# Performance work log

Measured on AMD Instinct MI355X. Metric: run time of the kernel, lower is better.

The kernel has to match this reference:

```python
import jax, jax.numpy as jnp
import numpy as np

N = 100000      # nodes
E = 1600000     # edges (avg degree 16)
F_NODE = 128
F_EDGE = 32
H = 32          # hidden size hard-coded in module


def setup_inputs() -> dict:
    key = jax.random.key(0)
    ks = jax.random.split(key, 16)
    w = lambda k, s: jax.random.normal(k, s, jnp.float32) * 0.05
    z = lambda n: jnp.zeros((n,), jnp.float32)
    return {
        "x": jax.random.normal(ks[0], (N, F_NODE), jnp.float32),
        "edge_index": jax.random.randint(ks[1], (2, E), 0, N),
        "edge_attr": jax.random.normal(ks[2], (E, F_EDGE), jnp.float32),
        "W_node": w(ks[3], (F_NODE, H)), "b_node": z(H),
        "W_edge": w(ks[4], (F_EDGE, H)), "b_edge": z(H),
        # TGCN: three GCNConv(32,32) gate convs + three Linear(64,32)
        "Wg_z": w(ks[5], (H, H)), "bg_z": z(H),
        "Wg_r": w(ks[6], (H, H)), "bg_r": z(H),
        "Wg_h": w(ks[7], (H, H)), "bg_h": z(H),
        "Wl_z": w(ks[8], (2 * H, H)), "bl_z": z(H),
        "Wl_r": w(ks[9], (2 * H, H)), "bl_r": z(H),
        "Wl_h": w(ks[10], (2 * H, H)), "bl_h": z(H),
        "W_out": w(ks[11], (3 * H, 1)), "b_out": z(1),
    }


def _gcn(x, row, col, dis, W, b, n):
    # GCNConv with added self-loops and symmetric normalization.
    xw = x @ W                                        # [N, H]
    msg = (dis[row] * dis[col])[:, None] * xw[row]    # [E, H]
    agg = jax.ops.segment_sum(msg, col, num_segments=n)
    agg = agg + (dis * dis)[:, None] * xw             # self-loop term
    return agg + b


def reference(x, edge_index, edge_attr, W_node, b_node, W_edge, b_edge,
              Wg_z, bg_z, Wg_r, bg_r, Wg_h, bg_h,
              Wl_z, bl_z, Wl_r, bl_r, Wl_h, bl_h, W_out, b_out):
    n = x.shape[0]
    row, col = edge_index[0], edge_index[1]
    x_enc = jax.nn.relu(x @ W_node + b_node)          # [N, 32]
    e_enc = jax.nn.relu(edge_attr @ W_edge + b_edge)  # [E, 32]

    # degree (target side) including self loop
    deg = jax.ops.segment_sum(jnp.ones_like(col, dtype=x.dtype), col,
                              num_segments=n) + 1.0
    dis = jax.lax.rsqrt(deg)

    h0 = jnp.zeros_like(x_enc)                        # TGCN initial state H=None -> zeros
    Z = jax.nn.sigmoid(
        jnp.concatenate([_gcn(x_enc, row, col, dis, Wg_z, bg_z, n), h0], 1) @ Wl_z + bl_z)
    R = jax.nn.sigmoid(
        jnp.concatenate([_gcn(x_enc, row, col, dis, Wg_r, bg_r, n), h0], 1) @ Wl_r + bl_r)
    Ht = jnp.tanh(
        jnp.concatenate([_gcn(x_enc, row, col, dis, Wg_h, bg_h, n), h0 * R], 1) @ Wl_h + bl_h)
    h = Z * h0 + (1.0 - Z) * Ht                       # [N, 32]

    # edge-level gather-concat + final linear -> [E, 1]
    edge_feat = jnp.concatenate([h[row], h[col], e_enc], axis=1)  # [E, 96]
    return edge_feat @ W_out + b_out
```

## Files before the change

kernel.cpp:

```cpp
#include <hip/hip_runtime.h>
#include <hip/hip_bf16.h>

#define F_NODE 128
#define BINCAP 64

__device__ __forceinline__ float bflo(unsigned int v) {
    return __uint_as_float(v << 16);
}
__device__ __forceinline__ float bfhi(unsigned int v) {
    return __uint_as_float(v & 0xffff0000u);
}
__device__ __forceinline__ unsigned short bfpack(float f) {
    __hip_bfloat16 b = __float2bfloat16(f);
    return *reinterpret_cast<unsigned short*>(&b);
}

__global__ void k_prep(const float* __restrict__ Wn,
                       const float* __restrict__ Wgz, const float* __restrict__ Wgh,
                       const float* __restrict__ Wlz, const float* __restrict__ Wlh,
                       const float* __restrict__ bgz, const float* __restrict__ bgh,
                       const float* __restrict__ blz, const float* __restrict__ blh,
                       const float* __restrict__ We,
                       float* __restrict__ Wnt, float* __restrict__ Mt,
                       float* __restrict__ cvec, float* __restrict__ Wet) {
    int tid = threadIdx.x;
    for (int j = tid; j < 32 * 128; j += 256) {
        int f = j >> 7, k = j & 127;
        Wnt[j] = Wn[k * 32 + f];
    }
    for (int j = tid; j < 64 * 32; j += 256) {
        int f2 = j >> 5, k = j & 31, f = f2 & 31;
        const float* G = (f2 < 32) ? Wgz : Wgh;
        const float* L = (f2 < 32) ? Wlz : Wlh;
        float s = 0.f;
        for (int q = 0; q < 32; ++q) s += G[k * 32 + q] * L[q * 32 + f];
        Mt[j] = s;
    }
    for (int j = tid; j < 64; j += 256) {
        int f = j & 31;
        const float* L  = (j < 32) ? Wlz : Wlh;
        const float* bg = (j < 32) ? bgz : bgh;
        const float* bl = (j < 32) ? blz : blh;
        float s = bl[f];
        for (int q = 0; q < 32; ++q) s += bg[q] * L[q * 32 + f];
        cvec[j] = s;
    }
    for (int j = tid; j < 32 * 32; j += 256) {
        int f = j >> 5, k = j & 31;
        Wet[j] = We[k * 32 + f];
    }
}

__global__ __launch_bounds__(256) void k_fat(
        const int* __restrict__ row, const int* __restrict__ col,
        int* __restrict__ cursor, int* __restrict__ bin,
        const float* __restrict__ ea, const float* __restrict__ Wet,
        const float* __restrict__ be, const float* __restrict__ Wout,
        const float* __restrict__ bout, float* __restrict__ out,
        const float* __restrict__ x, const float* __restrict__ bn,
        const float* __restrict__ Wnt, const float* __restrict__ Mt,
        __hip_bfloat16* __restrict__ ysb,
        int E, int N, int NB) {
    __shared__ float sW[1024];
    __shared__ float sb[32], sw3[32];
    __shared__ float sx[4][128];
    __shared__ float sxe[4][32];
    int role = blockIdx.x % 3;
    int chunk = blockIdx.x / 3;
    int tid = threadIdx.x;

    if (role == 0) {
        int e0 = chunk * 512 + tid, e1 = e0 + 256;
        if (e0 < E) {
            int r0 = row[e0];
            int c = col[e0];
            int p = atomicAdd(&cursor[c], 1);
            if (p < BINCAP)
                __builtin_nontemporal_store(r0, bin + ((size_t)c << 6) + p);
        }
        if (e1 < E) {
            int r1 = row[e1];
            int c = col[e1];
            int p = atomicAdd(&cursor[c], 1);
            if (p < BINCAP)
                __builtin_nontemporal_store(r1, bin + ((size_t)c << 6) + p);
        }
        return;
    }

    if (role == 1) {
        for (int j = tid; j < 1024; j += 256) sW[j] = Wet[j];
        if (tid < 32) { sb[tid] = be[tid]; sw3[tid] = Wout[64 + tid]; }
        __syncthreads();
        int e0 = chunk * 512 + tid, e1 = e0 + 256;
        bool v0 = e0 < E, v1 = e1 < E;
        const float4* ra = (const float4*)(ea + (size_t)(v0 ? e0 : 0) * 32);
        const float4* rb = (const float4*)(ea + (size_t)(v1 ? e1 : 0) * 32);
        float4 er0[8], er1[8];
        #pragma unroll
        for (int r = 0; r < 8; ++r) er0[r] = ra[r];
        #pragma unroll
        for (int r = 0; r < 8; ++r) er1[r] = rb[r];
        float p0 = 0.f, p1 = 0.f;
        #pragma unroll 4
        for (int f = 0; f < 32; ++f) {
            const float4* wf = (const float4*)(sW + f * 32);
            float s00 = 0.f, s01 = 0.f, s10 = 0.f, s11 = 0.f;
            #pragma unroll
            for (int k = 0; k < 8; k += 2) {
                float4 wa = wf[k], wb = wf[k + 1];
                float4 xa = er0[k], xb = er0[k + 1];
                float4 ya = er1[k], yb = er1[k + 1];
                s00 += xa.x*wa.x + xa.y*wa.y + xa.z*wa.z + xa.w*wa.w;
                s01 += xb.x*wb.x + xb.y*wb.y + xb.z*wb.z + xb.w*wb.w;
                s10 += ya.x*wa.x + ya.y*wa.y + ya.z*wa.z + ya.w*wa.w;
                s11 += yb.x*wb.x + yb.y*wb.y + yb.z*wb.z + yb.w*wb.w;
            }
            p0 += fmaxf(sb[f] + s00 + s01, 0.f) * sw3[f];
            p1 += fmaxf(sb[f] + s10 + s11, 0.f) * sw3[f];
        }
        float b0v = bout[0];
        if (v0) out[e0] = p0 + b0v;
        if (v1) out[e1] = p1 + b0v;
        return;
    }

    int w = tid >> 6, l = tid & 63;
    int f = l & 31, kh = l >> 5;

    float4 wreg[16];
    const float4* wp = (const float4*)(Wnt + f * 128 + kh * 64);
    #pragma unroll
    for (int r = 0; r < 16; ++r) wreg[r] = wp[r];
    float4 mreg[8];
    const float4* mp = (const float4*)(Mt + l * 32);
    #pragma unroll
    for (int r = 0; r < 8; ++r) mreg[r] = mp[r];
    float bnf = bn[f];

    int stride = NB * 4;
    int i = chunk * 4 + w;
    float2 xv = make_float2(0.f, 0.f);
    if (i < N) xv = ((const float2*)(x + (size_t)i * F_NODE))[l];

    for (; i < N; i += stride) {
        sx[w][2 * l]     = xv.x;
        sx[w][2 * l + 1] = xv.y;
        int inext = i + stride;
        if (inext < N) xv = ((const float2*)(x + (size_t)inext * F_NODE))[l];

        const float4* sxp = (const float4*)(&sx[w][kh * 64]);
        float a0 = 0.f, a1 = 0.f, a2 = 0.f, a3 = 0.f;
        #pragma unroll
        for (int r = 0; r < 16; r += 4) {
            float4 x0 = sxp[r], x1 = sxp[r + 1], x2 = sxp[r + 2], x3 = sxp[r + 3];
            float4 w0 = wreg[r], w1 = wreg[r + 1], w2 = wreg[r + 2], w3 = wreg[r + 3];
            a0 += x0.x*w0.x + x0.y*w0.y + x0.z*w0.z + x0.w*w0.w;
            a1 += x1.x*w1.x + x1.y*w1.y + x1.z*w1.z + x1.w*w1.w;
            a2 += x2.x*w2.x + x2.y*w2.y + x2.z*w2.z + x2.w*w2.w;
            a3 += x3.x*w3.x + x3.y*w3.y + x3.z*w3.z + x3.w*w3.w;
        }
        float acc = (a0 + a1) + (a2 + a3);
        acc += __shfl_xor(acc, 32);
        acc = fmaxf(acc + bnf, 0.f);
        if (l < 32) sxe[w][l] = acc;

        const float4* sep = (const float4*)(&sxe[w][0]);
        float b0 = 0.f, b1 = 0.f;
        #pragma unroll
        for (int r = 0; r < 8; r += 2) {
            float4 e0 = sep[r], e1 = sep[r + 1];
            float4 m0 = mreg[r], m1 = mreg[r + 1];
            b0 += e0.x*m0.x + e0.y*m0.y + e0.z*m0.z + e0.w*m0.w;
            b1 += e1.x*m1.x + e1.y*m1.y + e1.z*m1.z + e1.w*m1.w;
        }
        ysb[(size_t)i * 64 + l] = __float2bfloat16(b0 + b1);
    }
}

__global__ __launch_bounds__(256) void k_scale(
        uint4* __restrict__ ysb4, const int* __restrict__ cursor, int N) {
    int t = blockIdx.x * 256 + threadIdx.x;
    if (t >= N * 8) return;
    float d = rsqrtf((float)cursor[t >> 3] + 1.0f);
    uint4 v = ysb4[t];
    unsigned in[4] = {v.x, v.y, v.z, v.w};
    unsigned r[4];
    #pragma unroll
    for (int j = 0; j < 4; ++j) {
        unsigned short ul = bfpack(bflo(in[j]) * d);
        unsigned short uh = bfpack(bfhi(in[j]) * d);
        r[j] = (unsigned)ul | ((unsigned)uh << 16);
    }
    ysb4[t] = make_uint4(r[0], r[1], r[2], r[3]);
}

__global__ __launch_bounds__(256) void k_gather(
        const int* __restrict__ cursor, const int* __restrict__ bin,
        const unsigned short* __restrict__ ysb,
        const float* __restrict__ cvec, const float* __restrict__ Wout,
        float* __restrict__ hr, float* __restrict__ hc, int N) {
    int w = threadIdx.x >> 6, l = threadIdx.x & 63;
    int c = blockIdx.x * 4 + w;
    if (c >= N) return;
    int q = l & 15, s = l >> 4;

    int truec = cursor[c];
    float dc = rsqrtf((float)truec + 1.0f);
    int cnt = truec < BINCAP ? truec : BINCAP;
    const int* bp = bin + ((size_t)c << 6);
    int myr = (l < cnt) ? bp[l] : 0;

    float a0 = 0.f, a1 = 0.f, a2 = 0.f, a3 = 0.f;
    uint2 sv = *(const uint2*)(ysb + ((size_t)c << 6) + 4 * q);
    if (s == 0) {
        a0 = bflo(sv.x); a1 = bfhi(sv.x);
        a2 = bflo(sv.y); a3 = bfhi(sv.y);
    }
    for (int j = 0; j < cnt; j += 4) {
        int jj = j + s;
        if (jj < cnt) {
            int r = __shfl(myr, jj);
            uint2 v = *(const uint2*)(ysb + ((size_t)r << 6) + 4 * q);
            a0 += bflo(v.x); a1 += bfhi(v.x);
            a2 += bflo(v.y); a3 += bfhi(v.y);
        }
    }
    a0 += __shfl_xor(a0, 16); a1 += __shfl_xor(a1, 16);
    a2 += __shfl_xor(a2, 16); a3 += __shfl_xor(a3, 16);
    a0 += __shfl_xor(a0, 32); a1 += __shfl_xor(a1, 32);
    a2 += __shfl_xor(a2, 32); a3 += __shfl_xor(a3, 32);

    float4 cv = *(const float4*)(cvec + 4 * q);
    a0 = dc * a0 + cv.x; a1 = dc * a1 + cv.y;
    a2 = dc * a2 + cv.z; a3 = dc * a3 + cv.w;
    float v0, v1, v2, v3;
    if (q < 8) {
        v0 = 1.f / (1.f + __expf(-a0));
        v1 = 1.f / (1.f + __expf(-a1));
        v2 = 1.f / (1.f + __expf(-a2));
        v3 = 1.f / (1.f + __expf(-a3));
    } else {
        v0 = tanhf(a0); v1 = tanhf(a1); v2 = tanhf(a2); v3 = tanhf(a3);
    }
    float o0 = __shfl_xor(v0, 8), o1 = __shfl_xor(v1, 8);
    float o2 = __shfl_xor(v2, 8), o3 = __shfl_xor(v3, 8);
    float h0 = (1.f - v0) * o0, h1 = (1.f - v1) * o1;
    float h2 = (1.f - v2) * o2, h3 = (1.f - v3) * o3;
    float4 w0 = *(const float4*)(Wout + 4 * q);
    float4 w1 = *(const float4*)(Wout + 32 + 4 * q);
    float pr = h0*w0.x + h1*w0.y + h2*w0.z + h3*w0.w;
    float pc = h0*w1.x + h1*w1.y + h2*w1.z + h3*w1.w;
    #pragma unroll
    for (int m = 4; m >= 1; m >>= 1) {
        pr += __shfl_xor(pr, m);
        pc += __shfl_xor(pc, m);
    }
    if (l == 0) { hr[c] = pr; hc[c] = pc; }
}

__global__ __launch_bounds__(256) void k_edge_add(
        const int* __restrict__ row, const int* __restrict__ col,
        const float* __restrict__ hr, const float* __restrict__ hc,
        float* __restrict__ out, int E) {
    int e = blockIdx.x * 256 + threadIdx.x;
    if (e < E) out[e] += hr[row[e]] + hc[col[e]];
}

extern "C" void kernel_launch(void* const* d_in, const int* in_sizes, int n_in,
                              void* d_out, int out_size, void* d_ws, size_t ws_size,
                              hipStream_t stream) {
    const float* x    = (const float*)d_in[0];
    const int*   ei   = (const int*)  d_in[1];
    const float* ea   = (const float*)d_in[2];
    const float* Wn   = (const float*)d_in[3];
    const float* bn   = (const float*)d_in[4];
    const float* We   = (const float*)d_in[5];
    const float* be   = (const float*)d_in[6];
    const float* Wgz  = (const float*)d_in[7];
    const float* bgz  = (const float*)d_in[8];
    const float* Wgh  = (const float*)d_in[11];
    const float* bgh  = (const float*)d_in[12];
    const float* Wlz  = (const float*)d_in[13];
    const float* blz  = (const float*)d_in[14];
    const float* Wlh  = (const float*)d_in[17];
    const float* blh  = (const float*)d_in[18];
    const float* Wout = (const float*)d_in[19];
    const float* bout = (const float*)d_in[20];

    int N = in_sizes[0] / F_NODE;
    int E = in_sizes[1] / 2;
    const int* row = ei;
    const int* col = ei + E;

    float* ws    = (float*)d_ws;
    __hip_bfloat16* ysb = (__hip_bfloat16*)ws;
    int*   bin   = (int*)(ws + (size_t)32 * N);
    float* Wnt   = ws + (size_t)96 * N;
    float* Mt    = Wnt + 4096;
    float* Wet   = Mt + 2048;
    float* cvec  = Wet + 1024;
    float* hr    = cvec + 64;
    float* hc    = hr + N;
    int*   cursor= (int*)(hc + N);
    float* out   = (float*)d_out;

    hipMemsetAsync(cursor, 0, (size_t)N * sizeof(int), stream);

    k_prep<<<1, 256, 0, stream>>>(Wn, Wgz, Wgh, Wlz, Wlh, bgz, bgh, blz, blh, We,
                                  Wnt, Mt, cvec, Wet);
    int NB = (E + 511) / 512;
    k_fat<<<3 * NB, 256, 0, stream>>>(row, col, cursor, bin, ea, Wet, be, Wout,
                                      bout, out, x, bn, Wnt, Mt, ysb, E, N, NB);
    k_scale<<<(8 * N + 255) / 256, 256, 0, stream>>>((uint4*)ysb, cursor, N);
    k_gather<<<(N + 3) / 4, 256, 0, stream>>>(cursor, bin,
                                              (const unsigned short*)ysb,
                                              cvec, Wout, hr, hc, N);
    k_edge_add<<<(E + 255) / 256, 256, 0, stream>>>(row, col, hr, hc, out, E);
}
```

Baseline: 283.0 us.

## Replace per-node global atomic binning with two-level bucket binning in LDS

Edge binning by target node now first appends packed (row, local col) records into coarse 128-node buckets with a global atomic per bucket. A new per-bucket kernel then builds the per-node bins in shared memory and writes them out contiguously. That kernel also produces the degree cursor and applies the degree scaling, so the separate scale kernel is gone. The fused kernel's role split changes to 5 edge-encoder roles, 1 bucketing role and 1 node role per group of 7 blocks. The aim is fewer scattered global atomics and scattered bin writes, paid for with contention on the bucket counters, an extra bucket buffer and a fixed bucket capacity that could overflow on skewed graphs.

Measured after the change: 514.4 us. 1.82x slower.

```diff
diff --git a/kernel.cpp b/kernel.cpp
--- a/kernel.cpp
+++ b/kernel.cpp
@@ -51,47 +51,29 @@
     }
 }
 
-__global__ __launch_bounds__(256) void k_fat(
+__global__ __launch_bounds__(256) void k_fat3(
         const int* __restrict__ row, const int* __restrict__ col,
-        int* __restrict__ cursor, int* __restrict__ bin,
+        int* __restrict__ bcount, unsigned* __restrict__ buckets, int BCAP,
         const float* __restrict__ ea, const float* __restrict__ Wet,
         const float* __restrict__ be, const float* __restrict__ Wout,
         const float* __restrict__ bout, float* __restrict__ out,
         const float* __restrict__ x, const float* __restrict__ bn,
         const float* __restrict__ Wnt, const float* __restrict__ Mt,
         __hip_bfloat16* __restrict__ ysb,
-        int E, int N, int NB) {
+        int E, int N, int P) {
     __shared__ float sW[1024];
     __shared__ float sb[32], sw3[32];
     __shared__ float sx[4][128];
     __shared__ float sxe[4][32];
-    int role = blockIdx.x % 3;
-    int chunk = blockIdx.x / 3;
+    int role = blockIdx.x % 7;
+    int sub  = blockIdx.x / 7;
     int tid = threadIdx.x;
 
-    if (role == 0) {
-        int e0 = chunk * 512 + tid, e1 = e0 + 256;
-        if (e0 < E) {
-            int r0 = row[e0];
-            int c = col[e0];
-            int p = atomicAdd(&cursor[c], 1);
-            if (p < BINCAP)
-                __builtin_nontemporal_store(r0, bin + ((size_t)c << 6) + p);
-        }
-        if (e1 < E) {
-            int r1 = row[e1];
-            int c = col[e1];
-            int p = atomicAdd(&cursor[c], 1);
-            if (p < BINCAP)
-                __builtin_nontemporal_store(r1, bin + ((size_t)c << 6) + p);
-        }
-        return;
-    }
-
-    if (role == 1) {
+    if (role < 5) {
         for (int j = tid; j < 1024; j += 256) sW[j] = Wet[j];
         if (tid < 32) { sb[tid] = be[tid]; sw3[tid] = Wout[64 + tid]; }
         __syncthreads();
+        int chunk = sub * 5 + role;
         int e0 = chunk * 512 + tid, e1 = e0 + 256;
         bool v0 = e0 < E, v1 = e1 < E;
         const float4* ra = (const float4*)(ea + (size_t)(v0 ? e0 : 0) * 32);
@@ -125,6 +107,19 @@
         return;
     }
 
+    if (role == 5) {
+        int stride = P * 256;
+        for (int e = sub * 256 + tid; e < E; e += stride) {
+            int r = row[e];
+            int c = col[e];
+            int b = c >> 7;
+            unsigned rec = (unsigned)r | ((unsigned)(c & 127) << 20);
+            int p = atomicAdd(&bcount[b], 1);
+            if (p < BCAP) buckets[(size_t)b * BCAP + p] = rec;
+        }
+        return;
+    }
+
     int w = tid >> 6, l = tid & 63;
     int f = l & 31, kh = l >> 5;
 
@@ -138,8 +133,8 @@
     for (int r = 0; r < 8; ++r) mreg[r] = mp[r];
     float bnf = bn[f];
 
-    int stride = NB * 4;
-    int i = chunk * 4 + w;
+    int stride = P * 4;
+    int i = sub * 4 + w;
     float2 xv = make_float2(0.f, 0.f);
     if (i < N) xv = ((const float2*)(x + (size_t)i * F_NODE))[l];
 
@@ -178,21 +173,53 @@
     }
 }
 
-__global__ __launch_bounds__(256) void k_scale(
-        uint4* __restrict__ ysb4, const int* __restrict__ cursor, int N) {
-    int t = blockIdx.x * 256 + threadIdx.x;
-    if (t >= N * 8) return;
-    float d = rsqrtf((float)cursor[t >> 3] + 1.0f);
-    uint4 v = ysb4[t];
-    unsigned in[4] = {v.x, v.y, v.z, v.w};
-    unsigned r[4];
-    #pragma unroll
-    for (int j = 0; j < 4; ++j) {
-        unsigned short ul = bfpack(bflo(in[j]) * d);
-        unsigned short uh = bfpack(bfhi(in[j]) * d);
-        r[j] = (unsigned)ul | ((unsigned)uh << 16);
-    }
-    ysb4[t] = make_uint4(r[0], r[1], r[2], r[3]);
+__global__ __launch_bounds__(256) void k_bin(
+        const int* __restrict__ bcount, const unsigned* __restrict__ buckets,
+        int BCAP, int* __restrict__ bin, int* __restrict__ cursor,
+        uint4* __restrict__ ysb4, int N) {
+    __shared__ int lbin[128 * 64];
+    __shared__ int hist[128];
+    int b = blockIdx.x;
+    int tid = threadIdx.x;
+    int c0 = b << 7;
+    int nloc = N - c0; if (nloc > 128) nloc = 128;
+
+    for (int j = tid; j < 128; j += 256) hist[j] = 0;
+    __syncthreads();
+
+    int nb = bcount[b]; if (nb > BCAP) nb = BCAP;
+    const unsigned* bp = buckets + (size_t)b * BCAP;
+    for (int j = tid; j < nb; j += 256) {
+        unsigned v = bp[j];
+        int lc = v >> 20;
+        int r  = v & 0xFFFFFu;
+        int p = atomicAdd(&hist[lc], 1);
+        if (p < BINCAP) lbin[(lc << 6) + p] = r;
+    }
+    __syncthreads();
+
+    const uint4* src = (const uint4*)lbin;
+    uint4* dst = (uint4*)(bin + ((size_t)c0 << 6));
+    int nq = nloc << 4;
+    for (int j = tid; j < nq; j += 256) dst[j] = src[j];
+    if (tid < nloc) cursor[c0 + tid] = hist[tid];
+
+    int nv = nloc << 3;
+    for (int j = tid; j < nv; j += 256) {
+        int ln = j >> 3;
+        float d = rsqrtf((float)hist[ln] + 1.0f);
+        size_t idx = (((size_t)(c0 + ln)) << 3) + (j & 7);
+        uint4 v = ysb4[idx];
+        unsigned in[4] = {v.x, v.y, v.z, v.w};
+        unsigned r[4];
+        #pragma unroll
+        for (int k = 0; k < 4; ++k) {
+            unsigned short ul = bfpack(bflo(in[k]) * d);
+            unsigned short uh = bfpack(bfhi(in[k]) * d);
+            r[k] = (unsigned)ul | ((unsigned)uh << 16);
+        }
+        ysb4[idx] = make_uint4(r[0], r[1], r[2], r[3]);
+    }
 }
 
 __global__ __launch_bounds__(256) void k_gather(
@@ -293,26 +320,34 @@
     const int* row = ei;
     const int* col = ei + E;
 
+    int NBUCK = (N + 127) >> 7;
+    int BCAP  = E / NBUCK + E / (NBUCK * 4) + 512;
+
     float* ws    = (float*)d_ws;
     __hip_bfloat16* ysb = (__hip_bfloat16*)ws;
     int*   bin   = (int*)(ws + (size_t)32 * N);
-    float* Wnt   = ws + (size_t)96 * N;
+    unsigned* buckets = (unsigned*)(ws + (size_t)96 * N);
+    size_t BK = (size_t)NBUCK * BCAP;
+    float* Wnt   = ws + (size_t)96 * N + BK;
     float* Mt    = Wnt + 4096;
     float* Wet   = Mt + 2048;
     float* cvec  = Wet + 1024;
     float* hr    = cvec + 64;
     float* hc    = hr + N;
     int*   cursor= (int*)(hc + N);
+    int*   bcount= cursor + N;
     float* out   = (float*)d_out;
 
-    hipMemsetAsync(cursor, 0, (size_t)N * sizeof(int), stream);
+    hipMemsetAsync(bcount, 0, (size_t)NBUCK * sizeof(int), stream);
 
     k_prep<<<1, 256, 0, stream>>>(Wn, Wgz, Wgh, Wlz, Wlh, bgz, bgh, blz, blh, We,
                                   Wnt, Mt, cvec, Wet);
-    int NB = (E + 511) / 512;
-    k_fat<<<3 * NB, 256, 0, stream>>>(row, col, cursor, bin, ea, Wet, be, Wout,
-                                      bout, out, x, bn, Wnt, Mt, ysb, E, N, NB);
-    k_scale<<<(8 * N + 255) / 256, 256, 0, stream>>>((uint4*)ysb, cursor, N);
+    int P = (((E + 511) / 512) + 4) / 5;
+    k_fat3<<<7 * P, 256, 0, stream>>>(row, col, bcount, buckets, BCAP,
+                                      ea, Wet, be, Wout, bout, out,
+                                      x, bn, Wnt, Mt, ysb, E, N, P);
+    k_bin<<<NBUCK, 256, 0, stream>>>(bcount, buckets, BCAP, bin, cursor,
+                                     (uint4*)ysb, N);
     k_gather<<<(N + 3) / 4, 256, 0, stream>>>(cursor, bin,
                                               (const unsigned short*)ysb,
                                               cvec, Wout, hr, hc, N);
```
